# Optimization experiments

Hardware: AMD Instinct MI355X
Metric: run time of the kernel (lower is better)

The kernel has to match this reference:

```python
import jax, jax.numpy as jnp
import numpy as np

SEQ_LEN = 2048
NUM_HEADS = 16
DIM_EMB = 1024
DIM_HEAD = DIM_EMB // NUM_HEADS  # 64
DIM_K = DIM_EMB  # source scales by dim_k**-0.5 with dim_k defaulting to dim_emb
BASE = 10000
EPS = float(np.finfo(np.float32).eps)


def _rope_tables(seq_len, dim_head):
    idx = jnp.arange(seq_len, dtype=jnp.float32)
    scale = 1.0 / (BASE ** (jnp.arange(0, dim_head, 2, dtype=jnp.float32) / dim_head) + EPS)
    pos = jnp.outer(idx, scale)              # [S, dh/2]
    pos = jnp.concatenate([pos, pos], axis=-1)  # [S, dh]
    return jnp.cos(pos), jnp.sin(pos)


def _rotate_half(x):
    x1, x2 = x[..., : DIM_HEAD // 2], x[..., DIM_HEAD // 2 :]
    return jnp.concatenate([-x2, x1], axis=-1)


def _apply_rope(x, cos, sin):
    # x: [B, H, S, dh]; cos/sin: [S, dh]
    return x * cos[None, None] + _rotate_half(x) * sin[None, None]


def setup_inputs() -> dict:
    key = jax.random.key(0)
    k1, k2, k3 = jax.random.split(key, 3)
    x = jax.random.normal(k1, (2, SEQ_LEN, DIM_EMB), dtype=jnp.float32)
    Wqkv = jax.random.normal(k2, (DIM_EMB, 3 * DIM_EMB), dtype=jnp.float32) * 0.02
    Wout = jax.random.normal(k3, (DIM_EMB, DIM_EMB), dtype=jnp.float32) * 0.02
    return {"x": x, "Wqkv": Wqkv, "Wout": Wout}


def reference(x, Wqkv, Wout):
    B = x.shape[0]
    cos, sin = _rope_tables(SEQ_LEN, DIM_HEAD)
    qkv = x @ Wqkv  # [B, S, 3*E]
    q, k, v = jnp.split(qkv, 3, axis=-1)

    def to_heads(t):
        return t.reshape(B, SEQ_LEN, NUM_HEADS, DIM_HEAD).transpose(0, 2, 1, 3)

    q, k, v = to_heads(q), to_heads(k), to_heads(v)
    q = _apply_rope(q, cos, sin)
    k = _apply_rope(k, cos, sin)

    scores = jnp.einsum('bhsd,bhtd->bhst', q, k) * (DIM_K ** -0.5)
    causal_mask = jnp.triu(jnp.ones((SEQ_LEN, SEQ_LEN), dtype=bool), k=1)
    scores = jnp.where(causal_mask[None, None], -jnp.inf, scores)
    attn = jax.nn.softmax(scores, axis=-1)
    out = jnp.einsum('bhst,bhtd->bhsd', attn, v)
    out = out.transpose(0, 2, 1, 3).reshape(B, SEQ_LEN, DIM_EMB)
    return out @ Wout
```

## Files before the change

### kernel.cpp

```cpp
#include <hip/hip_runtime.h>

#define S_LEN 2048
#define NHEAD 16

using f32x4  = __attribute__((ext_vector_type(4))) float;
using f32x16 = __attribute__((ext_vector_type(16))) float;
using bf16x8 = __attribute__((ext_vector_type(8))) __bf16;

__device__ __forceinline__ unsigned short f2bf(float f) {
  union { float f; unsigned u; } v; v.f = f;
  unsigned r = v.u + 0x7FFFu + ((v.u >> 16) & 1u);
  return (unsigned short)(r >> 16);
}
__device__ __forceinline__ float bf2f(unsigned short h) {
  union { unsigned u; float f; } v; v.u = ((unsigned)h) << 16; return v.f;
}
__device__ __forceinline__ void unpack8(uint4 u, float x[8]) {
  x[0]=bf2f((unsigned short)(u.x&0xffff)); x[1]=bf2f((unsigned short)(u.x>>16));
  x[2]=bf2f((unsigned short)(u.y&0xffff)); x[3]=bf2f((unsigned short)(u.y>>16));
  x[4]=bf2f((unsigned short)(u.z&0xffff)); x[5]=bf2f((unsigned short)(u.z>>16));
  x[6]=bf2f((unsigned short)(u.w&0xffff)); x[7]=bf2f((unsigned short)(u.w>>16));
}
__device__ __forceinline__ uint4 pack8(const unsigned short o[8]) {
  uint4 u;
  u.x = (unsigned)o[0] | ((unsigned)o[1]<<16);
  u.y = (unsigned)o[2] | ((unsigned)o[3]<<16);
  u.z = (unsigned)o[4] | ((unsigned)o[5]<<16);
  u.w = (unsigned)o[6] | ((unsigned)o[7]<<16);
  return u;
}
__device__ __forceinline__ void gload16(const void* g, void* l) {
  __builtin_amdgcn_global_load_lds(
      (const __attribute__((address_space(1))) unsigned int*)g,
      (__attribute__((address_space(3))) unsigned int*)l, 16, 0, 0);
}
__device__ __forceinline__ float exp2_fast(float x) {
#if __has_builtin(__builtin_amdgcn_exp2f)
  return __builtin_amdgcn_exp2f(x);
#else
  return __expf(x * 0.6931471805599453f);
#endif
}
__device__ __forceinline__ void store_c(float* C, size_t off, float v) { C[off] = v; }
__device__ __forceinline__ void store_c(unsigned short* C, size_t off, float v) { C[off] = f2bf(v); }

__global__ __launch_bounds__(256) void k_cvt(const float* __restrict__ in,
                                             unsigned short* __restrict__ out, int n8) {
  int i = blockIdx.x * 256 + threadIdx.x;
  if (i >= n8) return;
  const float4* p = (const float4*)in + 2 * (size_t)i;
  float4 a = p[0], b = p[1];
  unsigned short o[8] = { f2bf(a.x), f2bf(a.y), f2bf(a.z), f2bf(a.w),
                          f2bf(b.x), f2bf(b.y), f2bf(b.z), f2bf(b.w) };
  ((uint4*)out)[i] = pack8(o);
}

__global__ __launch_bounds__(256) void k_transpose_cvt(const float* __restrict__ in,
                                                       unsigned short* __restrict__ out,
                                                       int R, int C) {
  __shared__ float T[64][65];
  int r0 = blockIdx.x * 64, c0 = blockIdx.y * 64;
  int tid = threadIdx.x;
#pragma unroll
  for (int i = 0; i < 16; ++i) {
    int idx = tid + i * 256;
    int r = idx >> 6, c = idx & 63;
    T[r][c] = in[(size_t)(r0 + r) * C + c0 + c];
  }
  __syncthreads();
#pragma unroll
  for (int i = 0; i < 8; ++i) {
    int idx = tid + i * 256;
    int co = idx >> 5, rp = (idx & 31) * 2;
    unsigned v = (unsigned)f2bf(T[rp][co]) | ((unsigned)f2bf(T[rp + 1][co]) << 16);
    *(unsigned*)&out[(size_t)(c0 + co) * R + r0 + rp] = v;
  }
}

template <typename OUT_T>
__global__ __launch_bounds__(256, 2) void k_gemm128(const unsigned short* __restrict__ A,
                                                    const unsigned short* __restrict__ Bt,
                                                    OUT_T* __restrict__ C,
                                                    int M, int N, int K) {
  __shared__ unsigned short As[2][128][64];
  __shared__ unsigned short Bs[2][128][64];
  const int tid = threadIdx.x;
  const int lane = tid & 63, w = tid >> 6;
  const int wm = w >> 1, wn = w & 1;
  const int li = lane & 15, g = lane >> 4;
  const int m0 = blockIdx.x * 128, n0 = blockIdx.y * 128;
  const int srow = w * 8 + (lane >> 3);
  const int scol = ((lane & 7) ^ ((lane >> 3) & 7)) * 8;

  f32x4 acc[4][4];
#pragma unroll
  for (int i = 0; i < 4; ++i)
#pragma unroll
    for (int j = 0; j < 4; ++j) acc[i][j] = (f32x4){0.f, 0.f, 0.f, 0.f};

  const int nt = K >> 6;

  auto stage_tile = [&](int kt) {
    int buf = kt & 1;
    const unsigned short* sa = A + (size_t)(m0 + srow) * K + kt * 64 + scol;
    const unsigned short* sb = Bt + (size_t)(n0 + srow) * K + kt * 64 + scol;
    char* da = (char*)&As[buf][srow][0];
    char* db = (char*)&Bs[buf][srow][0];
#pragma unroll
    for (int j = 0; j < 4; ++j) {
      gload16(sa + (size_t)(j * 32) * K, da + j * 32 * 128);
      gload16(sb + (size_t)(j * 32) * K, db + j * 32 * 128);
    }
  };

  stage_tile(0);

  for (int i = 0; i < nt; ++i) {
    if (i + 1 < nt) {
      stage_tile(i + 1);
      asm volatile("s_waitcnt vmcnt(8)" ::: "memory");
    } else {
      asm volatile("s_waitcnt vmcnt(0)" ::: "memory");
    }
    __builtin_amdgcn_s_barrier();
    asm volatile("" ::: "memory");
    const int buf = i & 1;
#pragma unroll
    for (int kk = 0; kk < 2; ++kk) {
      bf16x8 af[4], bfv[4];
      const int ps = ((kk << 2) | g) ^ (li & 7);
#pragma unroll
      for (int ii = 0; ii < 4; ++ii)
        af[ii] = *(const bf16x8*)&As[buf][wm * 64 + ii * 16 + li][ps * 8];
#pragma unroll
      for (int jj = 0; jj < 4; ++jj)
        bfv[jj] = *(const bf16x8*)&Bs[buf][wn * 64 + jj * 16 + li][ps * 8];
      __builtin_amdgcn_s_setprio(1);
#pragma unroll
      for (int ii = 0; ii < 4; ++ii)
#pragma unroll
        for (int jj = 0; jj < 4; ++jj)
          acc[ii][jj] = __builtin_amdgcn_mfma_f32_16x16x32_bf16(af[ii], bfv[jj],
                                                                acc[ii][jj], 0, 0, 0);
      __builtin_amdgcn_s_setprio(0);
    }
    asm volatile("" ::: "memory");
    __builtin_amdgcn_s_barrier();
    asm volatile("" ::: "memory");
  }

#pragma unroll
  for (int ii = 0; ii < 4; ++ii) {
    int row = m0 + wm * 64 + ii * 16 + g * 4;
#pragma unroll
    for (int jj = 0; jj < 4; ++jj) {
      int col = n0 + wn * 64 + jj * 16 + li;
#pragma unroll
      for (int r = 0; r < 4; ++r) store_c(C, (size_t)(row + r) * N + col, acc[ii][jj][r]);
    }
  }
}

__global__ __launch_bounds__(256) void k_rope_split(const unsigned short* __restrict__ qkv,
                                                    unsigned short* __restrict__ Qf,
                                                    unsigned short* __restrict__ Kf,
                                                    unsigned short* __restrict__ Vf) {
  int blk = blockIdx.x;
  int st = blk & 31, h = (blk >> 5) & 15, b = blk >> 9;
  int s0 = st * 64;
  int tid = threadIdx.x;
  int sl = tid >> 2, quad = tid & 3;
  int s = s0 + sl;
  int bh = b * NHEAD + h;
  int l31 = s & 31;
  int qt = s >> 5;
  int cq = quad >> 1, hiq = quad & 1;

  float cs[8], sn[8];
#pragma unroll
  for (int j = 0; j < 8; ++j) {
    int pr = quad * 8 + j;
    float e2 = exp2_fast((float)pr * 0.41524101f);
    float freq = 1.0f / (e2 + 1.1920928955078125e-07f);
    float x = (float)s * freq * 0.15915494309189535f;
    x -= floorf(x);
    float ang = x * 6.283185307179586f;
    sn[j] = __sinf(ang);
    cs[j] = __cosf(ang);
  }
  const unsigned short* row = qkv + (size_t)(b * S_LEN + s) * 3072;
  const float QSC = 0.04508422f;
  {
    float x1[8], x2[8];
    unpack8(*(const uint4*)&row[h * 64 + quad * 8], x1);
    unpack8(*(const uint4*)&row[h * 64 + 32 + quad * 8], x2);
    unsigned short o1[8], o2[8];
#pragma unroll
    for (int j = 0; j < 8; ++j) {
      o1[j] = f2bf((x1[j] * cs[j] - x2[j] * sn[j]) * QSC);
      o2[j] = f2bf((x2[j] * cs[j] + x1[j] * sn[j]) * QSC);
    }
    size_t base = ((size_t)bh * 64 + qt) * 4;
    int lane8 = (hiq * 32 + l31) * 8;
    *(uint4*)&Qf[(base + cq) * 512 + lane8] = pack8(o1);
    *(uint4*)&Qf[(base + 2 + cq) * 512 + lane8] = pack8(o2);
  }
  {
    float x1[8], x2[8];
    unpack8(*(const uint4*)&row[1024 + h * 64 + quad * 8], x1);
    unpack8(*(const uint4*)&row[1024 + h * 64 + 32 + quad * 8], x2);
    unsigned short o1[8], o2[8];
#pragma unroll
    for (int j = 0; j < 8; ++j) {
      o1[j] = f2bf(x1[j] * cs[j] - x2[j] * sn[j]);
      o2[j] = f2bf(x2[j] * cs[j] + x1[j] * sn[j]);
    }
    int lp = (l31 & 0x13) | ((l31 & 4) << 1) | ((l31 & 8) >> 1);
    size_t base = ((size_t)bh * 64 + qt) * 4;
    int lane8 = (hiq * 32 + lp) * 8;
    *(uint4*)&Kf[(base + cq) * 512 + lane8] = pack8(o1);
    *(uint4*)&Kf[(base + 2 + cq) * 512 + lane8] = pack8(o2);
  }
  __shared__ unsigned short Vl[64 * 72];
#pragma unroll
  for (int i = 0; i < 2; ++i) {
    int c = tid + i * 256;
    int r = c >> 3, c8 = (c & 7) * 8;
    *(uint4*)&Vl[r * 72 + c8] =
        *(const uint4*)&qkv[(size_t)(b * S_LEN + s0 + r) * 3072 + 2048 + h * 64 + c8];
  }
  __syncthreads();
  int d = tid >> 2, sc4 = tid & 3;
  unsigned o[8];
#pragma unroll
  for (int jj = 0; jj < 8; ++jj) {
    int sidx = sc4 * 16 + jj * 2;
    o[jj] = (unsigned)Vl[sidx * 72 + d] | ((unsigned)Vl[(sidx + 1) * 72 + d] << 16);
  }
  {
    int t = st * 2 + (sc4 >> 1);
    int c = ((d >> 5) << 1) + (sc4 & 1);
    size_t base = (((size_t)bh * 64 + t) * 4 + c) * 512;
    *(uint4*)&Vf[base + (d & 31) * 8]        = make_uint4(o[0], o[1], o[2], o[3]);
    *(uint4*)&Vf[base + (32 + (d & 31)) * 8] = make_uint4(o[4], o[5], o[6], o[7]);
  }
}

__global__ __launch_bounds__(256) void k_attn4(const unsigned short* __restrict__ Qf,
                                               const unsigned short* __restrict__ Kf,
                                               const unsigned short* __restrict__ Vf,
                                               unsigned short* __restrict__ O) {
  __shared__ float MBUF[3][2176];
  int bid = blockIdx.x;
  int i = (bid & 7) * 256 + (bid >> 3);
  int bh = i >> 6;
  int qt = 63 - (i & 63);
  int tid = threadIdx.x, w = tid >> 6, lane = tid & 63;
  int b = bh >> 4, h = bh & 15;
  int l31 = lane & 31, hi = lane >> 5;

  int n = qt + 1;
  int t0 = (w * n) >> 2, t1 = ((w + 1) * n) >> 2;

  const unsigned short* Kg = Kf + ((size_t)bh * 64) * 4 * 512 + lane * 8;
  const unsigned short* Vg = Vf + ((size_t)bh * 64) * 4 * 512 + lane * 8;

  float m_run = -1e30f, l_run = 0.f;
  f32x16 acc0, acc1;
#pragma unroll
  for (int r = 0; r < 16; ++r) { acc0[r] = 0.f; acc1[r] = 0.f; }

  if (t0 < t1) {
    const unsigned short* Qg = Qf + (((size_t)bh * 64 + qt) * 4) * 512 + lane * 8;
    bf16x8 qf[4];
#pragma unroll
    for (int c = 0; c < 4; ++c) qf[c] = *(const bf16x8*)(Qg + c * 512);

    auto loadK = [&](bf16x8 (&kf)[4], int t) {
      const unsigned short* kp = Kg + (size_t)t * 2048;
#pragma unroll
      for (int c = 0; c < 4; ++c) kf[c] = *(const bf16x8*)(kp + c * 512);
    };
    auto loadV = [&](bf16x8 (&vf)[4], int t) {
      const unsigned short* vp = Vg + (size_t)t * 2048;
#pragma unroll
      for (int c = 0; c < 4; ++c) vf[c] = *(const bf16x8*)(vp + c * 512);
    };
    auto step = [&](bf16x8 (&kf)[4], bf16x8 (&vf)[4], int t) {
      f32x16 s;
#pragma unroll
      for (int r = 0; r < 16; ++r) s[r] = 0.f;
      __builtin_amdgcn_s_setprio(1);
      s = __builtin_amdgcn_mfma_f32_32x32x16_bf16(kf[0], qf[0], s, 0, 0, 0);
      s = __builtin_amdgcn_mfma_f32_32x32x16_bf16(kf[1], qf[1], s, 0, 0, 0);
      s = __builtin_amdgcn_mfma_f32_32x32x16_bf16(kf[2], qf[2], s, 0, 0, 0);
      s = __builtin_amdgcn_mfma_f32_32x32x16_bf16(kf[3], qf[3], s, 0, 0, 0);
      __builtin_amdgcn_s_setprio(0);
      if (t == qt) {
#pragma unroll
        for (int r = 0; r < 16; ++r) {
          int kv = (r & 7) + 16 * (r >> 3) + 8 * hi;
          if (kv > l31) s[r] = -1e30f;
        }
      }
      float pmax;
      {
        float m0 = fmaxf(s[0], s[1]),   mm1 = fmaxf(s[2], s[3]);
        float m2 = fmaxf(s[4], s[5]),   m3 = fmaxf(s[6], s[7]);
        float m4 = fmaxf(s[8], s[9]),   m5 = fmaxf(s[10], s[11]);
        float m6 = fmaxf(s[12], s[13]), m7 = fmaxf(s[14], s[15]);
        m0 = fmaxf(m0, mm1); m2 = fmaxf(m2, m3); m4 = fmaxf(m4, m5); m6 = fmaxf(m6, m7);
        pmax = fmaxf(fmaxf(m0, m2), fmaxf(m4, m6));
      }
      if (__any(pmax > m_run + 8.0f)) {
        float pfull = fmaxf(pmax, __shfl_xor(pmax, 32));
        float mnew = fmaxf(m_run, pfull);
        float fac = exp2_fast(m_run - mnew);
        l_run *= fac;
#pragma unroll
        for (int r = 0; r < 16; ++r) { acc0[r] *= fac; acc1[r] *= fac; }
        m_run = mnew;
      }
#pragma unroll
      for (int r = 0; r < 16; ++r) s[r] = exp2_fast(s[r] - m_run);
      {
        float s0 = (s[0] + s[1]) + (s[2] + s[3]);
        float s1 = (s[4] + s[5]) + (s[6] + s[7]);
        float s2 = (s[8] + s[9]) + (s[10] + s[11]);
        float s3 = (s[12] + s[13]) + (s[14] + s[15]);
        l_run += (s0 + s1) + (s2 + s3);
      }
      bf16x8 pf0, pf1;
      {
        unsigned w0, w1, w2, w3;
        asm("v_cvt_pk_bf16_f32 %0, %1, %2" : "=v"(w0) : "v"(s[0]), "v"(s[1]));
        asm("v_cvt_pk_bf16_f32 %0, %1, %2" : "=v"(w1) : "v"(s[2]), "v"(s[3]));
        asm("v_cvt_pk_bf16_f32 %0, %1, %2" : "=v"(w2) : "v"(s[4]), "v"(s[5]));
        asm("v_cvt_pk_bf16_f32 %0, %1, %2" : "=v"(w3) : "v"(s[6]), "v"(s[7]));
        union { uint4 uu; bf16x8 v; } cv;
        cv.uu = make_uint4(w0, w1, w2, w3);
        pf0 = cv.v;
        asm("v_cvt_pk_bf16_f32 %0, %1, %2" : "=v"(w0) : "v"(s[8]), "v"(s[9]));
        asm("v_cvt_pk_bf16_f32 %0, %1, %2" : "=v"(w1) : "v"(s[10]), "v"(s[11]));
        asm("v_cvt_pk_bf16_f32 %0, %1, %2" : "=v"(w2) : "v"(s[12]), "v"(s[13]));
        asm("v_cvt_pk_bf16_f32 %0, %1, %2" : "=v"(w3) : "v"(s[14]), "v"(s[15]));
        cv.uu = make_uint4(w0, w1, w2, w3);
        pf1 = cv.v;
      }
      __builtin_amdgcn_s_setprio(1);
      acc0 = __builtin_amdgcn_mfma_f32_32x32x16_bf16(vf[0], pf0, acc0, 0, 0, 0);
      acc0 = __builtin_amdgcn_mfma_f32_32x32x16_bf16(vf[1], pf1, acc0, 0, 0, 0);
      acc1 = __builtin_amdgcn_mfma_f32_32x32x16_bf16(vf[2], pf0, acc1, 0, 0, 0);
      acc1 = __builtin_amdgcn_mfma_f32_32x32x16_bf16(vf[3], pf1, acc1, 0, 0, 0);
      __builtin_amdgcn_s_setprio(0);
    };

    bf16x8 kA[4], vA[4], kB[4], vB[4];
    loadK(kA, t0); loadV(vA, t0);
    int t = t0;
    while (true) {
      if (t + 1 < t1) { loadK(kB, t + 1); loadV(vB, t + 1); }
      step(kA, vA, t);
      ++t; if (t >= t1) break;
      if (t + 1 < t1) { loadK(kA, t + 1); loadV(vA, t + 1); }
      step(kB, vB, t);
      ++t; if (t >= t1) break;
    }
  }

  if (w != 0) {
    float* sb = &MBUF[w - 1][0];
#pragma unroll
    for (int r = 0; r < 16; ++r) {
      sb[r * 64 + lane] = acc0[r];
      sb[(16 + r) * 64 + lane] = acc1[r];
    }
    sb[2048 + lane] = m_run;
    sb[2112 + lane] = l_run;
  }
  __syncthreads();
  if (w == 0) {
    float m1 = MBUF[0][2048 + lane], m2 = MBUF[1][2048 + lane], m3 = MBUF[2][2048 + lane];
    float mF = fmaxf(fmaxf(m_run, m1), fmaxf(m2, m3));
    float f0 = exp2_fast(m_run - mF);
    float f1 = exp2_fast(m1 - mF);
    float f2 = exp2_fast(m2 - mF);
    float f3 = exp2_fast(m3 - mF);
    float lF = f0 * l_run + f1 * MBUF[0][2112 + lane] + f2 * MBUF[1][2112 + lane] +
               f3 * MBUF[2][2112 + lane];
    lF += __shfl_xor(lF, 32);
    float inv = 1.0f / lF;
    f32x16 o0, o1;
#pragma unroll
    for (int r = 0; r < 16; ++r) {
      o0[r] = (f0 * acc0[r] + f1 * MBUF[0][r * 64 + lane] + f2 * MBUF[1][r * 64 + lane] +
               f3 * MBUF[2][r * 64 + lane]) * inv;
      o1[r] = (f0 * acc1[r] + f1 * MBUF[0][(16 + r) * 64 + lane] +
               f2 * MBUF[1][(16 + r) * 64 + lane] + f3 * MBUF[2][(16 + r) * 64 + lane]) * inv;
    }
    unsigned short* ol = (unsigned short*)&MBUF[0][0];
#pragma unroll
    for (int dh = 0; dh < 2; ++dh) {
#pragma unroll
      for (int r = 0; r < 16; r += 2) {
        int dv = dh * 32 + (r & 3) + 8 * (r >> 2) + 4 * hi;
        float lo = dh ? o1[r] : o0[r];
        float hi_ = dh ? o1[r + 1] : o0[r + 1];
        unsigned uu;
        asm("v_cvt_pk_bf16_f32 %0, %1, %2" : "=v"(uu) : "v"(lo), "v"(hi_));
        *(unsigned*)&ol[l31 * 72 + dv] = uu;
      }
    }
    asm volatile("s_waitcnt lgkmcnt(0)" ::: "memory");
    int q0f = qt * 32;
    int q = lane >> 1, half = lane & 1;
    unsigned short* op = O + ((size_t)(b * S_LEN + q0f + q)) * 1024 + h * 64 + half * 32;
#pragma unroll
    for (int j = 0; j < 4; ++j)
      *(uint4*)(op + j * 8) = *(const uint4*)&ol[q * 72 + half * 32 + j * 8];
  }
}

extern "C" void kernel_launch(void* const* d_in, const int* in_sizes, int n_in,
                              void* d_out, int out_size, void* d_ws, size_t ws_size,
                              hipStream_t stream) {
  const float* x = (const float*)d_in[0];
  const float* Wqkv = (const float*)d_in[1];
  const float* Wout = (const float*)d_in[2];
  float* out = (float*)d_out;
  char* ws = (char*)d_ws;
  unsigned short* xb = (unsigned short*)(ws);
  unsigned short* WqkvT = (unsigned short*)(ws + ((size_t)8 << 20));
  unsigned short* WoutT = (unsigned short*)(ws + ((size_t)14 << 20));
  unsigned short* qkv = (unsigned short*)(ws + ((size_t)16 << 20));
  unsigned short* Qf = (unsigned short*)(ws + ((size_t)40 << 20));
  unsigned short* Kf = (unsigned short*)(ws + ((size_t)48 << 20));
  unsigned short* Vf = (unsigned short*)(ws + ((size_t)56 << 20));

  k_cvt<<<2048, 256, 0, stream>>>(x, xb, 4096 * 1024 / 8);
  k_transpose_cvt<<<dim3(16, 48), 256, 0, stream>>>(Wqkv, WqkvT, 1024, 3072);
  k_transpose_cvt<<<dim3(16, 16), 256, 0, stream>>>(Wout, WoutT, 1024, 1024);
  k_gemm128<unsigned short><<<dim3(32, 24), 256, 0, stream>>>(xb, WqkvT, qkv, 4096, 3072, 1024);
  k_rope_split<<<1024, 256, 0, stream>>>(qkv, Qf, Kf, Vf);
  k_attn4<<<2048, 256, 0, stream>>>(Qf, Kf, Vf, xb );
  k_gemm128<float><<<dim3(32, 8), 256, 0, stream>>>(xb, WoutT, out, 4096, 1024, 1024);
}
```

Before: 121.9 us.

## Fuse prep kernels, precompute RoPE table, restructure attention to share K/V tiles via LDS

Merges the x conversion and both weight transposes into one launch that also writes a cos/sin table, which k_rope_split now reads instead of recomputing. The table is staged in the output buffer, which the final GEMM later overwrites. The attention kernel changes from four waves splitting one query tile's KV range to four waves each owning a consecutive query tile. K/V tiles are streamed once per block into double-buffered LDS with global_load_lds, which removes the cross-wave softmax merge but adds two barriers per step and causal imbalance across waves.

```diff
diff --git a/kernel.cpp b/kernel.cpp
--- a/kernel.cpp
+++ b/kernel.cpp
@@ -44,23 +44,10 @@
 __device__ __forceinline__ void store_c(float* C, size_t off, float v) { C[off] = v; }
 __device__ __forceinline__ void store_c(unsigned short* C, size_t off, float v) { C[off] = f2bf(v); }
 
-__global__ __launch_bounds__(256) void k_cvt(const float* __restrict__ in,
-                                             unsigned short* __restrict__ out, int n8) {
-  int i = blockIdx.x * 256 + threadIdx.x;
-  if (i >= n8) return;
-  const float4* p = (const float4*)in + 2 * (size_t)i;
-  float4 a = p[0], b = p[1];
-  unsigned short o[8] = { f2bf(a.x), f2bf(a.y), f2bf(a.z), f2bf(a.w),
-                          f2bf(b.x), f2bf(b.y), f2bf(b.z), f2bf(b.w) };
-  ((uint4*)out)[i] = pack8(o);
-}
-
-__global__ __launch_bounds__(256) void k_transpose_cvt(const float* __restrict__ in,
-                                                       unsigned short* __restrict__ out,
-                                                       int R, int C) {
-  __shared__ float T[64][65];
-  int r0 = blockIdx.x * 64, c0 = blockIdx.y * 64;
-  int tid = threadIdx.x;
+__device__ __forceinline__ void transpose_body(const float* __restrict__ in,
+                                               unsigned short* __restrict__ out,
+                                               int R, int C, int r0, int c0,
+                                               float (*T)[65], int tid) {
 #pragma unroll
   for (int i = 0; i < 16; ++i) {
     int idx = tid + i * 256;
@@ -74,6 +61,45 @@
     int co = idx >> 5, rp = (idx & 31) * 2;
     unsigned v = (unsigned)f2bf(T[rp][co]) | ((unsigned)f2bf(T[rp + 1][co]) << 16);
     *(unsigned*)&out[(size_t)(c0 + co) * R + r0 + rp] = v;
+  }
+}
+
+__global__ __launch_bounds__(256) void k_prep(const float* __restrict__ x,
+                                              unsigned short* __restrict__ xb,
+                                              const float* __restrict__ Wqkv,
+                                              unsigned short* __restrict__ WqkvT,
+                                              const float* __restrict__ Wout,
+                                              unsigned short* __restrict__ WoutT,
+                                              float2* __restrict__ tab) {
+  __shared__ float T[64][65];
+  int blk = blockIdx.x;
+  int tid = threadIdx.x;
+  if (blk < 2048) {
+    int i = blk * 256 + tid;
+    const float4* p = (const float4*)x + 2 * (size_t)i;
+    float4 a = p[0], b = p[1];
+    unsigned short o[8] = { f2bf(a.x), f2bf(a.y), f2bf(a.z), f2bf(a.w),
+                            f2bf(b.x), f2bf(b.y), f2bf(b.z), f2bf(b.w) };
+    ((uint4*)xb)[i] = pack8(o);
+  } else if (blk < 2816) {
+    int b2 = blk - 2048;
+    transpose_body(Wqkv, WqkvT, 1024, 3072, (b2 & 15) * 64, (b2 >> 4) * 64, T, tid);
+  } else if (blk < 3072) {
+    int b3 = blk - 2816;
+    transpose_body(Wout, WoutT, 1024, 1024, (b3 & 15) * 64, (b3 >> 4) * 64, T, tid);
+  } else {
+    int gt = (blk - 3072) * 256 + tid;
+    int s = gt >> 2, quad = gt & 3;
+#pragma unroll
+    for (int j = 0; j < 8; ++j) {
+      int pr = quad * 8 + j;
+      float e2 = exp2_fast((float)pr * 0.41524101f);
+      float freq = 1.0f / (e2 + 1.1920928955078125e-07f);
+      float xx = (float)s * freq * 0.15915494309189535f;
+      xx -= floorf(xx);
+      float ang = xx * 6.283185307179586f;
+      tab[(size_t)s * 32 + pr] = make_float2(__cosf(ang), __sinf(ang));
+    }
   }
 }
 
@@ -162,6 +188,7 @@
 }
 
 __global__ __launch_bounds__(256) void k_rope_split(const unsigned short* __restrict__ qkv,
+                                                    const float2* __restrict__ tab,
                                                     unsigned short* __restrict__ Qf,
                                                     unsigned short* __restrict__ Kf,
                                                     unsigned short* __restrict__ Vf) {
@@ -177,16 +204,10 @@
   int cq = quad >> 1, hiq = quad & 1;
 
   float cs[8], sn[8];
-#pragma unroll
-  for (int j = 0; j < 8; ++j) {
-    int pr = quad * 8 + j;
-    float e2 = exp2_fast((float)pr * 0.41524101f);
-    float freq = 1.0f / (e2 + 1.1920928955078125e-07f);
-    float x = (float)s * freq * 0.15915494309189535f;
-    x -= floorf(x);
-    float ang = x * 6.283185307179586f;
-    sn[j] = __sinf(ang);
-    cs[j] = __cosf(ang);
+  {
+    const float2* tp = tab + (size_t)s * 32 + quad * 8;
+#pragma unroll
+    for (int j = 0; j < 8; ++j) { float2 t = tp[j]; cs[j] = t.x; sn[j] = t.y; }
   }
   const unsigned short* row = qkv + (size_t)(b * S_LEN + s) * 3072;
   const float QSC = 0.04508422f;
@@ -246,47 +267,88 @@
   }
 }
 
-__global__ __launch_bounds__(256) void k_attn4(const unsigned short* __restrict__ Qf,
+__global__ __launch_bounds__(256) void k_attn6(const unsigned short* __restrict__ Qf,
                                                const unsigned short* __restrict__ Kf,
                                                const unsigned short* __restrict__ Vf,
                                                unsigned short* __restrict__ O) {
-  __shared__ float MBUF[3][2176];
+  __shared__ unsigned short KS[2][4][512];
+  __shared__ unsigned short VS[2][4][512];
+  __shared__ unsigned short OL[4][32 * 72];
   int bid = blockIdx.x;
-  int i = (bid & 7) * 256 + (bid >> 3);
-  int bh = i >> 6;
-  int qt = 63 - (i & 63);
+  int i = (bid & 7) * 64 + (bid >> 3);
+  int bh = i >> 4;
+  int g = 15 - (i & 15);
   int tid = threadIdx.x, w = tid >> 6, lane = tid & 63;
   int b = bh >> 4, h = bh & 15;
   int l31 = lane & 31, hi = lane >> 5;
-
-  int n = qt + 1;
-  int t0 = (w * n) >> 2, t1 = ((w + 1) * n) >> 2;
-
-  const unsigned short* Kg = Kf + ((size_t)bh * 64) * 4 * 512 + lane * 8;
-  const unsigned short* Vg = Vf + ((size_t)bh * 64) * 4 * 512 + lane * 8;
+  int qt = 4 * g + w;
+  int q0 = qt * 32;
+  const int tmax = 4 * g + 3;
+
+  const unsigned short* Qg = Qf + (((size_t)bh * 64 + qt) * 4) * 512 + lane * 8;
+  bf16x8 qf[4];
+#pragma unroll
+  for (int c = 0; c < 4; ++c) qf[c] = *(const bf16x8*)(Qg + c * 512);
 
   float m_run = -1e30f, l_run = 0.f;
   f32x16 acc0, acc1;
 #pragma unroll
   for (int r = 0; r < 16; ++r) { acc0[r] = 0.f; acc1[r] = 0.f; }
 
-  if (t0 < t1) {
-    const unsigned short* Qg = Qf + (((size_t)bh * 64 + qt) * 4) * 512 + lane * 8;
-    bf16x8 qf[4];
-#pragma unroll
-    for (int c = 0; c < 4; ++c) qf[c] = *(const bf16x8*)(Qg + c * 512);
-
-    auto loadK = [&](bf16x8 (&kf)[4], int t) {
-      const unsigned short* kp = Kg + (size_t)t * 2048;
-#pragma unroll
-      for (int c = 0; c < 4; ++c) kf[c] = *(const bf16x8*)(kp + c * 512);
-    };
-    auto loadV = [&](bf16x8 (&vf)[4], int t) {
-      const unsigned short* vp = Vg + (size_t)t * 2048;
-#pragma unroll
-      for (int c = 0; c < 4; ++c) vf[c] = *(const bf16x8*)(vp + c * 512);
-    };
-    auto step = [&](bf16x8 (&kf)[4], bf16x8 (&vf)[4], int t) {
+  const unsigned short* Kg = Kf + ((size_t)bh * 64) * 2048 + (size_t)w * 512 + lane * 8;
+  const unsigned short* Vg = Vf + ((size_t)bh * 64) * 2048 + (size_t)w * 512 + lane * 8;
+  auto stage = [&](int buf, int t) {
+    gload16(Kg + (size_t)t * 2048, (char*)&KS[buf][w][0]);
+    gload16(Vg + (size_t)t * 2048, (char*)&VS[buf][w][0]);
+  };
+
+  auto rescale_check = [&](float pmax) {
+    if (__any(pmax > m_run + 8.0f)) {
+      float pfull = fmaxf(pmax, __shfl_xor(pmax, 32));
+      float mnew = fmaxf(m_run, pfull);
+      float fac = exp2_fast(m_run - mnew);
+      l_run *= fac;
+#pragma unroll
+      for (int r = 0; r < 16; ++r) { acc0[r] *= fac; acc1[r] *= fac; }
+      m_run = mnew;
+    }
+  };
+  auto cvt2 = [&](const f32x16& s, bf16x8& p0, bf16x8& p1) {
+    unsigned w0, w1, w2, w3;
+    asm("v_cvt_pk_bf16_f32 %0, %1, %2" : "=v"(w0) : "v"(s[0]), "v"(s[1]));
+    asm("v_cvt_pk_bf16_f32 %0, %1, %2" : "=v"(w1) : "v"(s[2]), "v"(s[3]));
+    asm("v_cvt_pk_bf16_f32 %0, %1, %2" : "=v"(w2) : "v"(s[4]), "v"(s[5]));
+    asm("v_cvt_pk_bf16_f32 %0, %1, %2" : "=v"(w3) : "v"(s[6]), "v"(s[7]));
+    union { uint4 uu; bf16x8 v; } cv;
+    cv.uu = make_uint4(w0, w1, w2, w3);
+    p0 = cv.v;
+    asm("v_cvt_pk_bf16_f32 %0, %1, %2" : "=v"(w0) : "v"(s[8]), "v"(s[9]));
+    asm("v_cvt_pk_bf16_f32 %0, %1, %2" : "=v"(w1) : "v"(s[10]), "v"(s[11]));
+    asm("v_cvt_pk_bf16_f32 %0, %1, %2" : "=v"(w2) : "v"(s[12]), "v"(s[13]));
+    asm("v_cvt_pk_bf16_f32 %0, %1, %2" : "=v"(w3) : "v"(s[14]), "v"(s[15]));
+    cv.uu = make_uint4(w0, w1, w2, w3);
+    p1 = cv.v;
+  };
+
+  stage(0, 0);
+
+  for (int t = 0; t <= tmax; ++t) {
+    const int buf = t & 1;
+    if (t < tmax) {
+      stage(buf ^ 1, t + 1);
+      asm volatile("s_waitcnt vmcnt(2)" ::: "memory");
+    } else {
+      asm volatile("s_waitcnt vmcnt(0)" ::: "memory");
+    }
+    asm volatile("" ::: "memory");
+    __builtin_amdgcn_s_barrier();
+    asm volatile("" ::: "memory");
+    if (t <= qt) {
+      bf16x8 kf[4], vf[4];
+#pragma unroll
+      for (int c = 0; c < 4; ++c) kf[c] = *(const bf16x8*)&KS[buf][c][lane * 8];
+#pragma unroll
+      for (int c = 0; c < 4; ++c) vf[c] = *(const bf16x8*)&VS[buf][c][lane * 8];
       f32x16 s;
 #pragma unroll
       for (int r = 0; r < 16; ++r) s[r] = 0.f;
@@ -312,15 +374,7 @@
         m0 = fmaxf(m0, mm1); m2 = fmaxf(m2, m3); m4 = fmaxf(m4, m5); m6 = fmaxf(m6, m7);
         pmax = fmaxf(fmaxf(m0, m2), fmaxf(m4, m6));
       }
-      if (__any(pmax > m_run + 8.0f)) {
-        float pfull = fmaxf(pmax, __shfl_xor(pmax, 32));
-        float mnew = fmaxf(m_run, pfull);
-        float fac = exp2_fast(m_run - mnew);
-        l_run *= fac;
-#pragma unroll
-        for (int r = 0; r < 16; ++r) { acc0[r] *= fac; acc1[r] *= fac; }
-        m_run = mnew;
-      }
+      rescale_check(pmax);
 #pragma unroll
       for (int r = 0; r < 16; ++r) s[r] = exp2_fast(s[r] - m_run);
       {
@@ -331,90 +385,38 @@
         l_run += (s0 + s1) + (s2 + s3);
       }
       bf16x8 pf0, pf1;
-      {
-        unsigned w0, w1, w2, w3;
-        asm("v_cvt_pk_bf16_f32 %0, %1, %2" : "=v"(w0) : "v"(s[0]), "v"(s[1]));
-        asm("v_cvt_pk_bf16_f32 %0, %1, %2" : "=v"(w1) : "v"(s[2]), "v"(s[3]));
-        asm("v_cvt_pk_bf16_f32 %0, %1, %2" : "=v"(w2) : "v"(s[4]), "v"(s[5]));
-        asm("v_cvt_pk_bf16_f32 %0, %1, %2" : "=v"(w3) : "v"(s[6]), "v"(s[7]));
-        union { uint4 uu; bf16x8 v; } cv;
-        cv.uu = make_uint4(w0, w1, w2, w3);
-        pf0 = cv.v;
-        asm("v_cvt_pk_bf16_f32 %0, %1, %2" : "=v"(w0) : "v"(s[8]), "v"(s[9]));
-        asm("v_cvt_pk_bf16_f32 %0, %1, %2" : "=v"(w1) : "v"(s[10]), "v"(s[11]));
-        asm("v_cvt_pk_bf16_f32 %0, %1, %2" : "=v"(w2) : "v"(s[12]), "v"(s[13]));
-        asm("v_cvt_pk_bf16_f32 %0, %1, %2" : "=v"(w3) : "v"(s[14]), "v"(s[15]));
-        cv.uu = make_uint4(w0, w1, w2, w3);
-        pf1 = cv.v;
-      }
+      cvt2(s, pf0, pf1);
       __builtin_amdgcn_s_setprio(1);
       acc0 = __builtin_amdgcn_mfma_f32_32x32x16_bf16(vf[0], pf0, acc0, 0, 0, 0);
       acc0 = __builtin_amdgcn_mfma_f32_32x32x16_bf16(vf[1], pf1, acc0, 0, 0, 0);
       acc1 = __builtin_amdgcn_mfma_f32_32x32x16_bf16(vf[2], pf0, acc1, 0, 0, 0);
       acc1 = __builtin_amdgcn_mfma_f32_32x32x16_bf16(vf[3], pf1, acc1, 0, 0, 0);
       __builtin_amdgcn_s_setprio(0);
-    };
-
-    bf16x8 kA[4], vA[4], kB[4], vB[4];
-    loadK(kA, t0); loadV(vA, t0);
-    int t = t0;
-    while (true) {
-      if (t + 1 < t1) { loadK(kB, t + 1); loadV(vB, t + 1); }
-      step(kA, vA, t);
-      ++t; if (t >= t1) break;
-      if (t + 1 < t1) { loadK(kA, t + 1); loadV(vA, t + 1); }
-      step(kB, vB, t);
-      ++t; if (t >= t1) break;
-    }
-  }
-
-  if (w != 0) {
-    float* sb = &MBUF[w - 1][0];
-#pragma unroll
-    for (int r = 0; r < 16; ++r) {
-      sb[r * 64 + lane] = acc0[r];
-      sb[(16 + r) * 64 + lane] = acc1[r];
-    }
-    sb[2048 + lane] = m_run;
-    sb[2112 + lane] = l_run;
-  }
-  __syncthreads();
-  if (w == 0) {
-    float m1 = MBUF[0][2048 + lane], m2 = MBUF[1][2048 + lane], m3 = MBUF[2][2048 + lane];
-    float mF = fmaxf(fmaxf(m_run, m1), fmaxf(m2, m3));
-    float f0 = exp2_fast(m_run - mF);
-    float f1 = exp2_fast(m1 - mF);
-    float f2 = exp2_fast(m2 - mF);
-    float f3 = exp2_fast(m3 - mF);
-    float lF = f0 * l_run + f1 * MBUF[0][2112 + lane] + f2 * MBUF[1][2112 + lane] +
-               f3 * MBUF[2][2112 + lane];
-    lF += __shfl_xor(lF, 32);
-    float inv = 1.0f / lF;
-    f32x16 o0, o1;
-#pragma unroll
-    for (int r = 0; r < 16; ++r) {
-      o0[r] = (f0 * acc0[r] + f1 * MBUF[0][r * 64 + lane] + f2 * MBUF[1][r * 64 + lane] +
-               f3 * MBUF[2][r * 64 + lane]) * inv;
-      o1[r] = (f0 * acc1[r] + f1 * MBUF[0][(16 + r) * 64 + lane] +
-               f2 * MBUF[1][(16 + r) * 64 + lane] + f3 * MBUF[2][(16 + r) * 64 + lane]) * inv;
-    }
-    unsigned short* ol = (unsigned short*)&MBUF[0][0];
-#pragma unroll
-    for (int dh = 0; dh < 2; ++dh) {
-#pragma unroll
-      for (int r = 0; r < 16; r += 2) {
-        int dv = dh * 32 + (r & 3) + 8 * (r >> 2) + 4 * hi;
-        float lo = dh ? o1[r] : o0[r];
-        float hi_ = dh ? o1[r + 1] : o0[r + 1];
-        unsigned uu;
-        asm("v_cvt_pk_bf16_f32 %0, %1, %2" : "=v"(uu) : "v"(lo), "v"(hi_));
-        *(unsigned*)&ol[l31 * 72 + dv] = uu;
-      }
-    }
-    asm volatile("s_waitcnt lgkmcnt(0)" ::: "memory");
-    int q0f = qt * 32;
+    }
+    asm volatile("" ::: "memory");
+    __builtin_amdgcn_s_barrier();
+    asm volatile("" ::: "memory");
+  }
+
+  float l_tot = l_run + __shfl_xor(l_run, 32);
+  float inv = 1.0f / l_tot;
+  unsigned short* ol = &OL[w][0];
+#pragma unroll
+  for (int dh = 0; dh < 2; ++dh) {
+#pragma unroll
+    for (int r = 0; r < 16; r += 2) {
+      int dv = dh * 32 + (r & 3) + 8 * (r >> 2) + 4 * hi;
+      float lo = (dh ? acc1[r] : acc0[r]) * inv;
+      float hi_ = (dh ? acc1[r + 1] : acc0[r + 1]) * inv;
+      unsigned uu;
+      asm("v_cvt_pk_bf16_f32 %0, %1, %2" : "=v"(uu) : "v"(lo), "v"(hi_));
+      *(unsigned*)&ol[l31 * 72 + dv] = uu;
+    }
+  }
+  asm volatile("s_waitcnt lgkmcnt(0)" ::: "memory");
+  {
     int q = lane >> 1, half = lane & 1;
-    unsigned short* op = O + ((size_t)(b * S_LEN + q0f + q)) * 1024 + h * 64 + half * 32;
+    unsigned short* op = O + ((size_t)(b * S_LEN + q0 + q)) * 1024 + h * 64 + half * 32;
 #pragma unroll
     for (int j = 0; j < 4; ++j)
       *(uint4*)(op + j * 8) = *(const uint4*)&ol[q * 72 + half * 32 + j * 8];
@@ -436,12 +438,11 @@
   unsigned short* Qf = (unsigned short*)(ws + ((size_t)40 << 20));
   unsigned short* Kf = (unsigned short*)(ws + ((size_t)48 << 20));
   unsigned short* Vf = (unsigned short*)(ws + ((size_t)56 << 20));
-
-  k_cvt<<<2048, 256, 0, stream>>>(x, xb, 4096 * 1024 / 8);
-  k_transpose_cvt<<<dim3(16, 48), 256, 0, stream>>>(Wqkv, WqkvT, 1024, 3072);
-  k_transpose_cvt<<<dim3(16, 16), 256, 0, stream>>>(Wout, WoutT, 1024, 1024);
+  float2* trig = (float2*)d_out;
+
+  k_prep<<<3104, 256, 0, stream>>>(x, xb, Wqkv, WqkvT, Wout, WoutT, trig);
   k_gemm128<unsigned short><<<dim3(32, 24), 256, 0, stream>>>(xb, WqkvT, qkv, 4096, 3072, 1024);
-  k_rope_split<<<1024, 256, 0, stream>>>(qkv, Qf, Kf, Vf);
-  k_attn4<<<2048, 256, 0, stream>>>(Qf, Kf, Vf, xb );
+  k_rope_split<<<1024, 256, 0, stream>>>(qkv, trig, Qf, Kf, Vf);
+  k_attn6<<<512, 256, 0, stream>>>(Qf, Kf, Vf, xb );
   k_gemm128<float><<<dim3(32, 8), 256, 0, stream>>>(xb, WoutT, out, 4096, 1024, 1024);
 }
```

Measured after the change: 141.4 us. 16.0% more time.
